# Kernel optimization log

Hardware: AMD Instinct MI355X
Metric: run time of the kernel (lower is better)

The kernel has to match this reference:

```python
import jax, jax.numpy as jnp
import numpy as np
import math

B, T, D, H, FFN_DIM, SE_HID = 16, 1024, 512, 8, 2048, 256
EPS = 1e-5  # torch LayerNorm default


def layer_norm(x, g, b):
    mu = jnp.mean(x, axis=-1, keepdims=True)
    var = jnp.mean((x - mu) ** 2, axis=-1, keepdims=True)
    return (x - mu) * jax.lax.rsqrt(var + EPS) * g + b


def setup_inputs() -> dict:
    key = jax.random.key(0)
    ks = jax.random.split(key, 8)
    s = 0.02
    return {
        "x": jax.random.normal(ks[0], (B, T, D), dtype=jnp.float32),
        "wq": jax.random.normal(ks[1], (D, D), dtype=jnp.float32) * s,
        "wk": jax.random.normal(ks[2], (D, D), dtype=jnp.float32) * s,
        "wv": jax.random.normal(ks[3], (D, D), dtype=jnp.float32) * s,
        "ln1_g": jnp.ones((D,), jnp.float32),
        "ln1_b": jnp.zeros((D,), jnp.float32),
        "se_w1": jax.random.normal(ks[4], (T, SE_HID), dtype=jnp.float32) * s,
        "se_w2": jax.random.normal(ks[5], (SE_HID, T), dtype=jnp.float32) * s,
        "ffn_g": jnp.ones((D,), jnp.float32),
        "ffn_b": jnp.zeros((D,), jnp.float32),
        "w1": jax.random.normal(ks[6], (D, FFN_DIM), dtype=jnp.float32) * s,
        "b1": jnp.zeros((FFN_DIM,), jnp.float32),
        "w2": jax.random.normal(ks[7], (FFN_DIM, D), dtype=jnp.float32) * s,
        "b2": jnp.zeros((D,), jnp.float32),
    }


def _forward(x, wq, wk, wv, ln1_g, ln1_b, se_w1, se_w2, ffn_g, ffn_b, w1, b1, w2, b2):
    # --- SE gate over the sequence axis: squeeze over feature dim D ---
    y = jnp.mean(x, axis=-1)                       # (B, T)
    gate = jax.nn.sigmoid(jax.nn.relu(y @ se_w1) @ se_w2)  # (B, T)
    x = x + x * gate[..., None]

    d = D // H
    n = layer_norm(x, ln1_g, ln1_b)
    q = (n @ wq).reshape(B, T, H, d)
    k = (n @ wk).reshape(B, T, H, d)
    v = (n @ wv).reshape(B, T, H, d)
    attn = jnp.einsum('bnhd,bmhd->bnmh', q, k) / math.sqrt(d)
    w = jax.nn.softmax(attn, axis=2)               # softmax over key dim m
    x = x + jnp.einsum('bnmh,bmhd->bnhd', w, v).reshape(B, T, D)

    # --- FFN (pre-norm, exact GELU as nn.GELU default) ---
    n2 = layer_norm(x, ffn_g, ffn_b)
    h = jax.nn.gelu(n2 @ w1 + b1, approximate=False)
    return x + (h @ w2 + b2)


def reference(x, wq, wk, wv, ln1_g, ln1_b, se_w1, se_w2, ffn_g, ffn_b, w1, b1, w2, b2):
    return _forward(x, wq, wk, wv, ln1_g, ln1_b, se_w1, se_w2, ffn_g, ffn_b, w1, b1, w2, b2)
```

## Files before the change

### kernel.cpp

```cpp
#include <hip/hip_runtime.h>

typedef unsigned int uint32;

using bf16x8 = __attribute__((ext_vector_type(8))) short;
using f32x4  = __attribute__((ext_vector_type(4))) float;

#define B_  16
#define T_  1024
#define D_  512
#define H_  8
#define HD_ 64
#define FFN_ 2048
#define SEH_ 256
#define EPS_ 1e-5f
#define PS_ 80

__device__ __forceinline__ ushort f2bf(float f) {
  uint32 x = __float_as_uint(f);
  return (ushort)((x + 0x7fffu + ((x >> 16) & 1u)) >> 16);
}
__device__ __forceinline__ float bf2f(ushort u) {
  return __uint_as_float(((uint32)u) << 16);
}
__device__ __forceinline__ float gelu_fast(float v) {
  float u = v * (0.7978845608f + 0.0356774081f * v * v);
  float e = __expf(2.0f * u);
  float t = 1.0f - 2.0f * __builtin_amdgcn_rcpf(e + 1.0f);
  return 0.5f * v * (1.0f + t);
}

__global__ __launch_bounds__(256) void cast_transpose_all_k(
    const float* __restrict__ wq, const float* __restrict__ wk,
    const float* __restrict__ wv, const float* __restrict__ w1,
    const float* __restrict__ w2, ushort* __restrict__ wqkvT,
    ushort* __restrict__ w1T, ushort* __restrict__ w2T) {
  __shared__ float tile[32][33];
  int bid = blockIdx.x;
  const float* W; ushort* WT; int K, N, bk, bn;
  if (bid < 768) {
    int w = bid >> 8, r = bid & 255;
    W = (w == 0) ? wq : (w == 1) ? wk : wv;
    WT = wqkvT + (size_t)w * 512 * 512;
    K = 512; N = 512; bk = (r >> 4) * 32; bn = (r & 15) * 32;
  } else if (bid < 1792) {
    int r = bid - 768;
    W = w1; WT = w1T; K = 512; N = 2048; bk = (r >> 6) * 32; bn = (r & 63) * 32;
  } else {
    int r = bid - 1792;
    W = w2; WT = w2T; K = 2048; N = 512; bk = (r >> 4) * 32; bn = (r & 15) * 32;
  }
  int lx = threadIdx.x & 31;
  int ly = threadIdx.x >> 5;
  #pragma unroll
  for (int i = ly; i < 32; i += 8)
    tile[i][lx] = W[(size_t)(bk + i) * N + bn + lx];
  __syncthreads();
  #pragma unroll
  for (int i = ly; i < 32; i += 8)
    WT[(size_t)(bn + i) * K + bk + lx] = f2bf(tile[lx][i]);
}

__global__ __launch_bounds__(256) void se_rowmean_k(const float* __restrict__ x,
                                                    float* __restrict__ y) {
  int row  = blockIdx.x * 4 + (threadIdx.x >> 6);
  int lane = threadIdx.x & 63;
  const float4* p = (const float4*)(x + (size_t)row * D_);
  float4 a = p[lane * 2];
  float4 b = p[lane * 2 + 1];
  float s = a.x + a.y + a.z + a.w + b.x + b.y + b.z + b.w;
  #pragma unroll
  for (int m = 1; m < 64; m <<= 1) s += __shfl_xor(s, m);
  if (lane == 0) y[row] = s * (1.0f / D_);
}

__global__ __launch_bounds__(256) void se_mlp1_k(const float* __restrict__ y,
                                                 const float* __restrict__ w1,
                                                 float* __restrict__ z) {
  __shared__ float yb[T_];
  __shared__ float part[8][32];
  int b = blockIdx.x, jt = blockIdx.y;
  int tid = threadIdx.x;
  #pragma unroll
  for (int i = 0; i < 4; i++) yb[tid + i * 256] = y[(size_t)b * T_ + tid + i * 256];
  __syncthreads();
  int tj = tid & 31, tk = tid >> 5;
  int j = jt * 32 + tj;
  const float* wp = w1 + (size_t)(tk * 128) * SEH_ + j;
  const float* yp = yb + tk * 128;
  float a0 = 0.f, a1 = 0.f, a2 = 0.f, a3 = 0.f;
  #pragma unroll
  for (int t = 0; t < 128; t += 4) {
    a0 += yp[t]     * wp[(t)     * SEH_];
    a1 += yp[t + 1] * wp[(t + 1) * SEH_];
    a2 += yp[t + 2] * wp[(t + 2) * SEH_];
    a3 += yp[t + 3] * wp[(t + 3) * SEH_];
  }
  part[tk][tj] = (a0 + a1) + (a2 + a3);
  __syncthreads();
  if (tid < 32) {
    float s = 0.f;
    #pragma unroll
    for (int k = 0; k < 8; k++) s += part[k][tid];
    z[(size_t)b * SEH_ + jt * 32 + tid] = fmaxf(s, 0.f);
  }
}

__global__ __launch_bounds__(256) void se_mlp2_k(const float* __restrict__ z,
                                                 const float* __restrict__ w2,
                                                 float* __restrict__ gate) {
  __shared__ float zb[SEH_];
  __shared__ float part[2][128];
  int b = blockIdx.x, bt = blockIdx.y;
  int tid = threadIdx.x;
  zb[tid & 255] = z[(size_t)b * SEH_ + (tid & 255)];
  __syncthreads();
  int tt = tid & 127, tk = tid >> 7;
  int t = bt * 128 + tt;
  const float* wp = w2 + (size_t)(tk * 128) * T_ + t;
  const float* zp = zb + tk * 128;
  float a0 = 0.f, a1 = 0.f, a2 = 0.f, a3 = 0.f;
  #pragma unroll
  for (int j = 0; j < 128; j += 4) {
    a0 += zp[j]     * wp[(j)     * T_];
    a1 += zp[j + 1] * wp[(j + 1) * T_];
    a2 += zp[j + 2] * wp[(j + 2) * T_];
    a3 += zp[j + 3] * wp[(j + 3) * T_];
  }
  part[tk][tt] = (a0 + a1) + (a2 + a3);
  __syncthreads();
  if (tid < 128) {
    float s = part[0][tid] + part[1][tid];
    gate[(size_t)b * T_ + bt * 128 + tid] = 1.0f / (1.0f + __expf(-s));
  }
}

__global__ __launch_bounds__(256) void gate_ln1_k(
    const float* __restrict__ x, const float* __restrict__ gate,
    const float* __restrict__ g, const float* __restrict__ beta,
    float* __restrict__ x1, ushort* __restrict__ nbuf) {
  int rid  = blockIdx.x * 4 + (threadIdx.x >> 6);
  int lane = threadIdx.x & 63;
  const float4* xr = (const float4*)(x + (size_t)rid * D_);
  float4 a = xr[lane * 2];
  float4 b = xr[lane * 2 + 1];
  float gv = 1.0f + gate[rid];
  a.x *= gv; a.y *= gv; a.z *= gv; a.w *= gv;
  b.x *= gv; b.y *= gv; b.z *= gv; b.w *= gv;
  float4* x1r = (float4*)(x1 + (size_t)rid * D_);
  x1r[lane * 2]     = a;
  x1r[lane * 2 + 1] = b;
  float s  = a.x + a.y + a.z + a.w + b.x + b.y + b.z + b.w;
  float ss = a.x*a.x + a.y*a.y + a.z*a.z + a.w*a.w + b.x*b.x + b.y*b.y + b.z*b.z + b.w*b.w;
  #pragma unroll
  for (int m = 1; m < 64; m <<= 1) { s += __shfl_xor(s, m); ss += __shfl_xor(ss, m); }
  float mu   = s * (1.0f / D_);
  float var  = ss * (1.0f / D_) - mu * mu;
  float rstd = rsqrtf(var + EPS_);
  const float4* gp = (const float4*)g;
  const float4* bp = (const float4*)beta;
  float4 g0 = gp[lane * 2], g1 = gp[lane * 2 + 1];
  float4 b0 = bp[lane * 2], b1 = bp[lane * 2 + 1];
  union { uint4 v; ushort u[8]; } pk;
  pk.u[0] = f2bf((a.x - mu) * rstd * g0.x + b0.x);
  pk.u[1] = f2bf((a.y - mu) * rstd * g0.y + b0.y);
  pk.u[2] = f2bf((a.z - mu) * rstd * g0.z + b0.z);
  pk.u[3] = f2bf((a.w - mu) * rstd * g0.w + b0.w);
  pk.u[4] = f2bf((b.x - mu) * rstd * g1.x + b1.x);
  pk.u[5] = f2bf((b.y - mu) * rstd * g1.y + b1.y);
  pk.u[6] = f2bf((b.z - mu) * rstd * g1.z + b1.z);
  pk.u[7] = f2bf((b.w - mu) * rstd * g1.w + b1.w);
  *(uint4*)(nbuf + (size_t)rid * D_ + lane * 8) = pk.v;
}

__global__ __launch_bounds__(256) void ln2_k(
    const float* __restrict__ x2, const float* __restrict__ g,
    const float* __restrict__ beta, ushort* __restrict__ nbuf) {
  int rid  = blockIdx.x * 4 + (threadIdx.x >> 6);
  int lane = threadIdx.x & 63;
  const float4* xr = (const float4*)(x2 + (size_t)rid * D_);
  float4 a = xr[lane * 2];
  float4 b = xr[lane * 2 + 1];
  float s  = a.x + a.y + a.z + a.w + b.x + b.y + b.z + b.w;
  float ss = a.x*a.x + a.y*a.y + a.z*a.z + a.w*a.w + b.x*b.x + b.y*b.y + b.z*b.z + b.w*b.w;
  #pragma unroll
  for (int m = 1; m < 64; m <<= 1) { s += __shfl_xor(s, m); ss += __shfl_xor(ss, m); }
  float mu   = s * (1.0f / D_);
  float var  = ss * (1.0f / D_) - mu * mu;
  float rstd = rsqrtf(var + EPS_);
  const float4* gp = (const float4*)g;
  const float4* bp = (const float4*)beta;
  float4 g0 = gp[lane * 2], g1 = gp[lane * 2 + 1];
  float4 b0 = bp[lane * 2], b1 = bp[lane * 2 + 1];
  union { uint4 v; ushort u[8]; } pk;
  pk.u[0] = f2bf((a.x - mu) * rstd * g0.x + b0.x);
  pk.u[1] = f2bf((a.y - mu) * rstd * g0.y + b0.y);
  pk.u[2] = f2bf((a.z - mu) * rstd * g0.z + b0.z);
  pk.u[3] = f2bf((a.w - mu) * rstd * g0.w + b0.w);
  pk.u[4] = f2bf((b.x - mu) * rstd * g1.x + b1.x);
  pk.u[5] = f2bf((b.y - mu) * rstd * g1.y + b1.y);
  pk.u[6] = f2bf((b.z - mu) * rstd * g1.z + b1.z);
  pk.u[7] = f2bf((b.w - mu) * rstd * g1.w + b1.w);
  *(uint4*)(nbuf + (size_t)rid * D_ + lane * 8) = pk.v;
}

__global__ __launch_bounds__(256) void gemm128_k(
    const ushort* __restrict__ A, const ushort* __restrict__ BT,
    int M, int N, int K,
    const float* __restrict__ bias, const float* __restrict__ resid,
    ushort* __restrict__ outB, ushort* __restrict__ outB2,
    ushort* __restrict__ vTout, float* __restrict__ outF, int epi) {
  __shared__ ushort As[128 * 32];
  __shared__ ushort Bs[128 * 32];
  int tid  = threadIdx.x;
  int wave = tid >> 6;
  int lane = tid & 63;
  int quad = lane >> 4;
  int l15  = lane & 15;
  int wm   = wave >> 1;
  int wn   = wave & 1;
  int n0 = blockIdx.x * 128;
  int m0 = blockIdx.y * 128;

  f32x4 acc[4][4];
  #pragma unroll
  for (int mt = 0; mt < 4; mt++)
    #pragma unroll
    for (int nt = 0; nt < 4; nt++) acc[mt][nt] = (f32x4){0.f, 0.f, 0.f, 0.f};

  int lrow = lane >> 2;
  int lcol = (lane & 3) * 8;

  const ushort* Ag = A  + (size_t)(m0 + wave * 32 + lrow) * K + lcol;
  const ushort* Bg = BT + (size_t)(n0 + wave * 32 + lrow) * K + lcol;
  ushort* AsW = As + (wave * 32) * 32;
  ushort* BsW = Bs + (wave * 32) * 32;

  for (int kk = 0; kk < K; kk += 32) {
    __builtin_amdgcn_global_load_lds(
        (const __attribute__((address_space(1))) void*)(Ag + kk),
        (__attribute__((address_space(3))) void*)AsW, 16, 0, 0);
    __builtin_amdgcn_global_load_lds(
        (const __attribute__((address_space(1))) void*)(Ag + kk + 16 * (size_t)K),
        (__attribute__((address_space(3))) void*)(AsW + 16 * 32), 16, 0, 0);
    __builtin_amdgcn_global_load_lds(
        (const __attribute__((address_space(1))) void*)(Bg + kk),
        (__attribute__((address_space(3))) void*)BsW, 16, 0, 0);
    __builtin_amdgcn_global_load_lds(
        (const __attribute__((address_space(1))) void*)(Bg + kk + 16 * (size_t)K),
        (__attribute__((address_space(3))) void*)(BsW + 16 * 32), 16, 0, 0);
    __syncthreads();
    bf16x8 af[4], bfr[4];
    #pragma unroll
    for (int mt = 0; mt < 4; mt++)
      af[mt] = *(const bf16x8*)(As + (wm * 64 + mt * 16 + l15) * 32 + quad * 8);
    #pragma unroll
    for (int nt = 0; nt < 4; nt++)
      bfr[nt] = *(const bf16x8*)(Bs + (wn * 64 + nt * 16 + l15) * 32 + quad * 8);
    #pragma unroll
    for (int mt = 0; mt < 4; mt++)
      #pragma unroll
      for (int nt = 0; nt < 4; nt++)
        acc[mt][nt] = __builtin_amdgcn_mfma_f32_16x16x32_bf16(af[mt], bfr[nt], acc[mt][nt], 0, 0, 0);
    __syncthreads();
  }

  if (epi == 1) {
    #pragma unroll
    for (int nt = 0; nt < 4; nt++) {
      int n = n0 + wn * 64 + nt * 16 + l15;
      float bv = bias[n];
      #pragma unroll
      for (int mt = 0; mt < 4; mt++) {
        #pragma unroll
        for (int r = 0; r < 4; r++) {
          int m = m0 + wm * 64 + mt * 16 + quad * 4 + r;
          outB[(size_t)m * N + n] = f2bf(gelu_fast(acc[mt][nt][r] + bv));
        }
      }
    }
  } else if (epi == 2) {
    #pragma unroll
    for (int nt = 0; nt < 4; nt++) {
      int n = n0 + wn * 64 + nt * 16 + l15;
      float bv = bias[n];
      #pragma unroll
      for (int mt = 0; mt < 4; mt++) {
        #pragma unroll
        for (int r = 0; r < 4; r++) {
          int m = m0 + wm * 64 + mt * 16 + quad * 4 + r;
          size_t idx = (size_t)m * N + n;
          outF[idx] = acc[mt][nt][r] + bv + resid[idx];
        }
      }
    }
  } else {
    if (n0 < 1024) {
      ushort* dst = (n0 < 512) ? outB : outB2;
      float scl = (n0 < 512) ? 0.125f : 1.0f;
      int nb = n0 & 511;
      #pragma unroll
      for (int nt = 0; nt < 4; nt++) {
        int n = nb + wn * 64 + nt * 16 + l15;
        #pragma unroll
        for (int mt = 0; mt < 4; mt++) {
          #pragma unroll
          for (int r = 0; r < 4; r++) {
            int m = m0 + wm * 64 + mt * 16 + quad * 4 + r;
            dst[(size_t)m * 512 + n] = f2bf(acc[mt][nt][r] * scl);
          }
        }
      }
    } else {
      #pragma unroll
      for (int nt = 0; nt < 4; nt++) {
        int n = (n0 - 1024) + wn * 64 + nt * 16 + l15;
        int h = n >> 6, d = n & 63;
        #pragma unroll
        for (int mt = 0; mt < 4; mt++) {
          int mb = m0 + wm * 64 + mt * 16 + quad * 4;
          int bb = mb >> 10, t = mb & 1023;
          ushort4 pk;
          pk.x = f2bf(acc[mt][nt][0]);
          pk.y = f2bf(acc[mt][nt][1]);
          pk.z = f2bf(acc[mt][nt][2]);
          pk.w = f2bf(acc[mt][nt][3]);
          *(ushort4*)(vTout + (((size_t)bb * 8 + h) * 64 + d) * 1024 + t) = pk;
        }
      }
    }
  }
}

__global__ __launch_bounds__(256) void attn_k(
    const ushort* __restrict__ q, const ushort* __restrict__ k,
    const ushort* __restrict__ vT, const float* __restrict__ x1,
    float* __restrict__ out) {
  __shared__ ushort Ks[64 * PS_];
  __shared__ ushort Vs[64 * PS_];
  __shared__ ushort Ps[128 * PS_];
  int blk = blockIdx.x;
  int qt = blk & 7;
  int h  = (blk >> 3) & 7;
  int b  = blk >> 6;
  int t0 = qt * 128;
  int tid  = threadIdx.x;
  int wave = tid >> 6;
  int lane = tid & 63;
  int quad = lane >> 4;
  int l15  = lane & 15;

  const ushort* qp0 = q + ((size_t)(b * T_ + t0 + wave * 16 + l15)) * D_ + h * HD_;
  const ushort* qp1 = qp0 + (size_t)64 * D_;
  bf16x8 aq0 = *(const bf16x8*)(qp0 + quad * 8);
  bf16x8 aq1 = *(const bf16x8*)(qp0 + 32 + quad * 8);
  bf16x8 aq2 = *(const bf16x8*)(qp1 + quad * 8);
  bf16x8 aq3 = *(const bf16x8*)(qp1 + 32 + quad * 8);

  int srow = tid >> 2;
  int scol = (tid & 3) * 16;

  float l_part[2][4] = {{0.f, 0.f, 0.f, 0.f}, {0.f, 0.f, 0.f, 0.f}};
  f32x4 o0[4], o1[4];
  #pragma unroll
  for (int dt = 0; dt < 4; dt++) {
    o0[dt] = (f32x4){0.f, 0.f, 0.f, 0.f};
    o1[dt] = (f32x4){0.f, 0.f, 0.f, 0.f};
  }

  const ushort* vTb = vT + ((size_t)(b * 8 + h) * 64 + srow) * 1024 + scol;

  for (int kt = 0; kt < 16; kt++) {
    size_t kgbase = ((size_t)(b * T_ + kt * 64 + srow)) * D_ + h * HD_ + scol;
    uint4 ku0 = *(const uint4*)(k + kgbase);
    uint4 ku1 = *(const uint4*)(k + kgbase + 8);
    const ushort* vp = vTb + kt * 64;
    uint4 vv0 = *(const uint4*)(vp);
    uint4 vv1 = *(const uint4*)(vp + 8);

    __syncthreads();

    *(uint4*)(Ks + srow * PS_ + scol)     = ku0;
    *(uint4*)(Ks + srow * PS_ + scol + 8) = ku1;
    *(uint4*)(Vs + srow * PS_ + scol)     = vv0;
    *(uint4*)(Vs + srow * PS_ + scol + 8) = vv1;

    __syncthreads();

    f32x4 s0[4], s1[4];
    #pragma unroll
    for (int nt = 0; nt < 4; nt++) {
      bf16x8 bk0 = *(const bf16x8*)(Ks + (nt * 16 + l15) * PS_ + quad * 8);
      bf16x8 bk1 = *(const bf16x8*)(Ks + (nt * 16 + l15) * PS_ + 32 + quad * 8);
      f32x4 z = (f32x4){0.f, 0.f, 0.f, 0.f};
      s0[nt] = __builtin_amdgcn_mfma_f32_16x16x32_bf16(aq0, bk0, z, 0, 0, 0);
      s0[nt] = __builtin_amdgcn_mfma_f32_16x16x32_bf16(aq1, bk1, s0[nt], 0, 0, 0);
      s1[nt] = __builtin_amdgcn_mfma_f32_16x16x32_bf16(aq2, bk0, z, 0, 0, 0);
      s1[nt] = __builtin_amdgcn_mfma_f32_16x16x32_bf16(aq3, bk1, s1[nt], 0, 0, 0);
    }

    #pragma unroll
    for (int nt = 0; nt < 4; nt++) {
      int pcol = nt * 16 + l15;
      int prow0 = (wave * 16 + quad * 4) * PS_ + pcol;
      #pragma unroll
      for (int r = 0; r < 4; r++) {
        float p0 = __expf(s0[nt][r]);
        float p1 = __expf(s1[nt][r]);
        l_part[0][r] += p0;
        l_part[1][r] += p1;
        Ps[prow0 + r * PS_]            = f2bf(p0);
        Ps[prow0 + (64 + r) * PS_]     = f2bf(p1);
      }
    }

    bf16x8 ap0 = *(const bf16x8*)(Ps + (wave * 16 + l15) * PS_ + quad * 8);
    bf16x8 ap1 = *(const bf16x8*)(Ps + (wave * 16 + l15) * PS_ + 32 + quad * 8);
    bf16x8 ap2 = *(const bf16x8*)(Ps + (64 + wave * 16 + l15) * PS_ + quad * 8);
    bf16x8 ap3 = *(const bf16x8*)(Ps + (64 + wave * 16 + l15) * PS_ + 32 + quad * 8);
    #pragma unroll
    for (int dt = 0; dt < 4; dt++) {
      bf16x8 bv0 = *(const bf16x8*)(Vs + (dt * 16 + l15) * PS_ + quad * 8);
      bf16x8 bv1 = *(const bf16x8*)(Vs + (dt * 16 + l15) * PS_ + 32 + quad * 8);
      o0[dt] = __builtin_amdgcn_mfma_f32_16x16x32_bf16(ap0, bv0, o0[dt], 0, 0, 0);
      o0[dt] = __builtin_amdgcn_mfma_f32_16x16x32_bf16(ap1, bv1, o0[dt], 0, 0, 0);
      o1[dt] = __builtin_amdgcn_mfma_f32_16x16x32_bf16(ap2, bv0, o1[dt], 0, 0, 0);
      o1[dt] = __builtin_amdgcn_mfma_f32_16x16x32_bf16(ap3, bv1, o1[dt], 0, 0, 0);
    }
  }

  #pragma unroll
  for (int s = 0; s < 2; s++) {
    f32x4* oo = s ? o1 : o0;
    #pragma unroll
    for (int r = 0; r < 4; r++) {
      float l = l_part[s][r];
      l += __shfl_xor(l, 1);
      l += __shfl_xor(l, 2);
      l += __shfl_xor(l, 4);
      l += __shfl_xor(l, 8);
      float inv = 1.0f / l;
      int qrow = t0 + s * 64 + wave * 16 + quad * 4 + r;
      size_t base = ((size_t)(b * T_ + qrow)) * D_ + h * HD_;
      #pragma unroll
      for (int dt = 0; dt < 4; dt++) {
        size_t idx = base + dt * 16 + l15;
        out[idx] = x1[idx] + oo[dt][r] * inv;
      }
    }
  }
}

extern "C" void kernel_launch(void* const* d_in, const int* in_sizes, int n_in,
                              void* d_out, int out_size, void* d_ws, size_t ws_size,
                              hipStream_t stream) {
  (void)in_sizes; (void)n_in; (void)out_size; (void)ws_size;
  const float* x     = (const float*)d_in[0];
  const float* wq    = (const float*)d_in[1];
  const float* wk    = (const float*)d_in[2];
  const float* wv    = (const float*)d_in[3];
  const float* ln1_g = (const float*)d_in[4];
  const float* ln1_b = (const float*)d_in[5];
  const float* se_w1 = (const float*)d_in[6];
  const float* se_w2 = (const float*)d_in[7];
  const float* ffn_g = (const float*)d_in[8];
  const float* ffn_b = (const float*)d_in[9];
  const float* w1    = (const float*)d_in[10];
  const float* b1    = (const float*)d_in[11];
  const float* w2    = (const float*)d_in[12];
  const float* b2    = (const float*)d_in[13];
  float* out = (float*)d_out;
  char* ws = (char*)d_ws;

  constexpr size_t X1_OFF   = 0;
  constexpr size_t N_OFF    = 33554432;
  constexpr size_t Q_OFF    = 50331648;
  constexpr size_t K_OFF    = 67108864;
  constexpr size_t V_OFF    = 83886080;
  constexpr size_t H_OFF    = 50331648;
  constexpr size_t WQKV_OFF = 117440512;
  constexpr size_t W1T_OFF  = 119013376;
  constexpr size_t W2T_OFF  = 121110528;
  constexpr size_t Y_OFF    = 123207680;
  constexpr size_t Z_OFF    = 123273216;
  constexpr size_t GATE_OFF = 123289600;

  float*  x1    = (float*)(ws + X1_OFF);
  ushort* nbuf  = (ushort*)(ws + N_OFF);
  ushort* qb    = (ushort*)(ws + Q_OFF);
  ushort* kb    = (ushort*)(ws + K_OFF);
  ushort* vT    = (ushort*)(ws + V_OFF);
  ushort* hb    = (ushort*)(ws + H_OFF);
  ushort* wqkvT = (ushort*)(ws + WQKV_OFF);
  ushort* w1T   = (ushort*)(ws + W1T_OFF);
  ushort* w2T   = (ushort*)(ws + W2T_OFF);
  float*  yv    = (float*)(ws + Y_OFF);
  float*  zv    = (float*)(ws + Z_OFF);
  float*  gate  = (float*)(ws + GATE_OFF);

  const int M = B_ * T_;

  cast_transpose_all_k<<<2816, 256, 0, stream>>>(wq, wk, wv, w1, w2, wqkvT, w1T, w2T);

  se_rowmean_k<<<M / 4, 256, 0, stream>>>(x, yv);
  se_mlp1_k<<<dim3(B_, 8), 256, 0, stream>>>(yv, se_w1, zv);
  se_mlp2_k<<<dim3(B_, 8), 256, 0, stream>>>(zv, se_w2, gate);

  gate_ln1_k<<<M / 4, 256, 0, stream>>>(x, gate, ln1_g, ln1_b, x1, nbuf);

  gemm128_k<<<dim3(1536 / 128, M / 128), 256, 0, stream>>>(
      nbuf, wqkvT, M, 1536, D_, nullptr, nullptr, qb, kb, vT, nullptr, 3);

  attn_k<<<B_ * H_ * (T_ / 128), 256, 0, stream>>>(qb, kb, vT, x1, out);

  ln2_k<<<M / 4, 256, 0, stream>>>(out, ffn_g, ffn_b, nbuf);

  gemm128_k<<<dim3(FFN_ / 128, M / 128), 256, 0, stream>>>(
      nbuf, w1T, M, FFN_, D_, b1, nullptr, hb, nullptr, nullptr, nullptr, 1);
  gemm128_k<<<dim3(D_ / 128, M / 128), 256, 0, stream>>>(
      hb, w2T, M, D_, FFN_, b2, out, nullptr, nullptr, nullptr, out, 2);
}
```

Baseline: 378.6 us.

## Double-buffer GEMM LDS tiles and remap blocks for XCD-aware L2 locality

```diff
diff --git a/kernel.cpp b/kernel.cpp
--- a/kernel.cpp
+++ b/kernel.cpp
@@ -14,6 +14,9 @@
 #define SEH_ 256
 #define EPS_ 1e-5f
 #define PS_ 80
+
+#define AS1 __attribute__((address_space(1)))
+#define AS3 __attribute__((address_space(3)))
 
 __device__ __forceinline__ ushort f2bf(float f) {
   uint32 x = __float_as_uint(f);
@@ -209,8 +212,8 @@
     const float* __restrict__ bias, const float* __restrict__ resid,
     ushort* __restrict__ outB, ushort* __restrict__ outB2,
     ushort* __restrict__ vTout, float* __restrict__ outF, int epi) {
-  __shared__ ushort As[128 * 32];
-  __shared__ ushort Bs[128 * 32];
+  __shared__ ushort As[2 * 128 * 32];
+  __shared__ ushort Bs[2 * 128 * 32];
   int tid  = threadIdx.x;
   int wave = tid >> 6;
   int lane = tid & 63;
@@ -218,8 +221,13 @@
   int l15  = lane & 15;
   int wm   = wave >> 1;
   int wn   = wave & 1;
-  int n0 = blockIdx.x * 128;
-  int m0 = blockIdx.y * 128;
+
+  int nbk = N >> 7;
+  int bid = blockIdx.x;
+  int xcd = bid & 7;
+  int s   = bid >> 3;
+  int n0  = (s % nbk) << 7;
+  int m0  = ((s / nbk) * 8 + xcd) << 7;
 
   f32x4 acc[4][4];
   #pragma unroll
@@ -235,27 +243,36 @@
   ushort* AsW = As + (wave * 32) * 32;
   ushort* BsW = Bs + (wave * 32) * 32;
 
-  for (int kk = 0; kk < K; kk += 32) {
-    __builtin_amdgcn_global_load_lds(
-        (const __attribute__((address_space(1))) void*)(Ag + kk),
-        (__attribute__((address_space(3))) void*)AsW, 16, 0, 0);
-    __builtin_amdgcn_global_load_lds(
-        (const __attribute__((address_space(1))) void*)(Ag + kk + 16 * (size_t)K),
-        (__attribute__((address_space(3))) void*)(AsW + 16 * 32), 16, 0, 0);
-    __builtin_amdgcn_global_load_lds(
-        (const __attribute__((address_space(1))) void*)(Bg + kk),
-        (__attribute__((address_space(3))) void*)BsW, 16, 0, 0);
-    __builtin_amdgcn_global_load_lds(
-        (const __attribute__((address_space(1))) void*)(Bg + kk + 16 * (size_t)K),
-        (__attribute__((address_space(3))) void*)(BsW + 16 * 32), 16, 0, 0);
+#define STAGE(IT, BUF)                                                         \
+  do {                                                                         \
+    int _ko = (IT) * 32;                                                       \
+    ushort* _a = AsW + (BUF) * (128 * 32);                                     \
+    ushort* _b = BsW + (BUF) * (128 * 32);                                     \
+    __builtin_amdgcn_global_load_lds((const AS1 void*)(Ag + _ko),              \
+                                     (AS3 void*)_a, 16, 0, 0);                 \
+    __builtin_amdgcn_global_load_lds((const AS1 void*)(Ag + _ko + 16 * (size_t)K), \
+                                     (AS3 void*)(_a + 16 * 32), 16, 0, 0);     \
+    __builtin_amdgcn_global_load_lds((const AS1 void*)(Bg + _ko),              \
+                                     (AS3 void*)_b, 16, 0, 0);                 \
+    __builtin_amdgcn_global_load_lds((const AS1 void*)(Bg + _ko + 16 * (size_t)K), \
+                                     (AS3 void*)(_b + 16 * 32), 16, 0, 0);     \
+  } while (0)
+
+  int niter = K >> 5;
+  STAGE(0, 0);
+  for (int i = 0; i < niter; i++) {
+    int cur = i & 1;
     __syncthreads();
+    if (i + 1 < niter) STAGE(i + 1, cur ^ 1);
+    const ushort* Asb = As + cur * (128 * 32);
+    const ushort* Bsb = Bs + cur * (128 * 32);
     bf16x8 af[4], bfr[4];
     #pragma unroll
     for (int mt = 0; mt < 4; mt++)
-      af[mt] = *(const bf16x8*)(As + (wm * 64 + mt * 16 + l15) * 32 + quad * 8);
+      af[mt] = *(const bf16x8*)(Asb + (wm * 64 + mt * 16 + l15) * 32 + quad * 8);
     #pragma unroll
     for (int nt = 0; nt < 4; nt++)
-      bfr[nt] = *(const bf16x8*)(Bs + (wn * 64 + nt * 16 + l15) * 32 + quad * 8);
+      bfr[nt] = *(const bf16x8*)(Bsb + (wn * 64 + nt * 16 + l15) * 32 + quad * 8);
     #pragma unroll
     for (int mt = 0; mt < 4; mt++)
       #pragma unroll
@@ -263,6 +280,7 @@
         acc[mt][nt] = __builtin_amdgcn_mfma_f32_16x16x32_bf16(af[mt], bfr[nt], acc[mt][nt], 0, 0, 0);
     __syncthreads();
   }
+#undef STAGE
 
   if (epi == 1) {
     #pragma unroll
@@ -507,15 +525,15 @@
 
   gate_ln1_k<<<M / 4, 256, 0, stream>>>(x, gate, ln1_g, ln1_b, x1, nbuf);
 
-  gemm128_k<<<dim3(1536 / 128, M / 128), 256, 0, stream>>>(
+  gemm128_k<<<(M / 128) * (1536 / 128), 256, 0, stream>>>(
       nbuf, wqkvT, M, 1536, D_, nullptr, nullptr, qb, kb, vT, nullptr, 3);
 
   attn_k<<<B_ * H_ * (T_ / 128), 256, 0, stream>>>(qb, kb, vT, x1, out);
 
   ln2_k<<<M / 4, 256, 0, stream>>>(out, ffn_g, ffn_b, nbuf);
 
-  gemm128_k<<<dim3(FFN_ / 128, M / 128), 256, 0, stream>>>(
+  gemm128_k<<<(M / 128) * (FFN_ / 128), 256, 0, stream>>>(
       nbuf, w1T, M, FFN_, D_, b1, nullptr, hb, nullptr, nullptr, nullptr, 1);
-  gemm128_k<<<dim3(D_ / 128, M / 128), 256, 0, stream>>>(
+  gemm128_k<<<(M / 128) * (D_ / 128), 256, 0, stream>>>(
       hb, w2T, M, D_, FFN_, b2, out, nullptr, nullptr, nullptr, out, 2);
 }
```

New measurement: 365.4 us. 1.04x faster.
